# Kernel optimization log

Hardware: AMD Instinct MI355X
Metric: run time of the kernel (lower is better)

## Reference

```python
import jax, jax.numpy as jnp
import numpy as np

TOTAL = 131072          # total sentences
DIM = 690               # relation_dim (PCNN: 3*230)
NUM_CLASSES = 53        # NYT-10 relations
TOTAL_TYPE = 324        # type_num^2 = 18^2
NUM_BAGS = 8192
ALPHA = 0.9


def setup_inputs() -> dict:
    key = jax.random.key(0)
    ks = jax.random.split(key, 8)
    x = jax.random.normal(ks[0], (TOTAL, DIM), dtype=jnp.float32)
    # strictly increasing bag boundaries: scope[0]=0, scope[-1]=TOTAL, all bags non-empty
    rng = np.random.default_rng(0)
    cuts = np.sort(rng.choice(np.arange(1, TOTAL), NUM_BAGS - 1, replace=False))
    input_scope = jnp.asarray(np.concatenate([[0], cuts, [TOTAL]]), dtype=jnp.int32)
    type_label = jax.random.randint(ks[1], (TOTAL,), 0, TOTAL_TYPE, dtype=jnp.int32)
    query = jax.random.randint(ks[2], (TOTAL,), 0, NUM_CLASSES, dtype=jnp.int32)
    # learned parameters (xavier-ish scale)
    rel_scale = (6.0 / (NUM_CLASSES + DIM)) ** 0.5
    typ_scale = (6.0 / (TOTAL_TYPE + DIM)) ** 0.5
    lin_scale = (6.0 / (DIM + TOTAL_TYPE)) ** 0.5
    relation_weight = jax.random.uniform(ks[3], (NUM_CLASSES, DIM), jnp.float32, -rel_scale, rel_scale)
    type_weight = jax.random.uniform(ks[4], (TOTAL_TYPE, DIM), jnp.float32, -typ_scale, typ_scale)
    bias = jax.random.normal(ks[5], (NUM_CLASSES,), dtype=jnp.float32)
    liner_w = jax.random.uniform(ks[6], (TOTAL_TYPE, DIM), jnp.float32, -lin_scale, lin_scale)
    liner_b = jnp.zeros((TOTAL_TYPE,), dtype=jnp.float32)
    return {
        "x": x, "input_scope": input_scope, "type_label": type_label, "query": query,
        "relation_weight": relation_weight, "type_weight": type_weight, "bias": bias,
        "liner_w": liner_w, "liner_b": liner_b,
    }


def reference(x, input_scope, type_label, query, relation_weight, type_weight, bias, liner_w, liner_b):
    # ---- soft_type (beta != 0 branch) ----
    type_logits = jax.nn.softmax(x @ liner_w.T + liner_b, axis=1)          # [total, T2]
    max_scores = jnp.max(type_logits, axis=1, keepdims=True)               # [total, 1]
    one_hot = jax.nn.one_hot(type_label, TOTAL_TYPE, dtype=type_logits.dtype)
    nscore = type_logits + ALPHA * max_scores * one_hot
    soft_label = jnp.argmax(nscore, axis=1)                                # [total]

    # ---- _train_logits: per-sentence attention logits ----
    xt = x + type_weight[soft_label]                                       # [total, D]
    att = jnp.sum(xt * relation_weight[query], axis=1)                     # [total]

    # ---- bag-wise segment softmax + weighted sum over scopes ----
    seg = jnp.searchsorted(input_scope, jnp.arange(TOTAL), side="right") - 1  # [total] bag ids
    m = jax.ops.segment_max(att, seg, num_segments=NUM_BAGS)               # [bags]
    p = jnp.exp(att - m[seg])
    s = jax.ops.segment_sum(p, seg, num_segments=NUM_BAGS)                 # [bags]
    score = p / s[seg]                                                     # [total]
    bag_repre = jax.ops.segment_sum(score[:, None] * x, seg, num_segments=NUM_BAGS)  # [bags, D]

    # ---- _logits ----
    logits = bag_repre @ relation_weight.T + bias                          # [bags, C]
    return logits, type_logits
```

## Files before the change

kernel.cpp:

```cpp
#include <hip/hip_runtime.h>
#include <hip/hip_bf16.h>

#define TOTAL   131072
#define DIMK    690
#define KPAD    704
#define KSTEPS  22
#define NCLASS  53
#define NTYPE   324
#define NCOLS   377
#define NPAD    384
#define NBAGS   8192
#define ALPHA   0.9f
#define TAU     1e-5f
#define FLAGCAP 32768
#define ZS      388

typedef short  bf16x8 __attribute__((ext_vector_type(8)));
typedef float  f32x4  __attribute__((ext_vector_type(4)));

__device__ __forceinline__ unsigned short bf16_rne(float f) {
    unsigned int u = __float_as_uint(f);
    u = (u + 0x7fffu + ((u >> 16) & 1u)) >> 16;
    return (unsigned short)u;
}
__device__ __forceinline__ float bf16f(unsigned short h) {
    return __uint_as_float(((unsigned int)h) << 16);
}

__global__ __launch_bounds__(256) void k_pack(const float* __restrict__ liner_w,
                                              const float* __restrict__ rel_w,
                                              unsigned short* __restrict__ whP,
                                              unsigned short* __restrict__ wlP) {
    const int id = blockIdx.x * 256 + threadIdx.x;
    if (id >= NPAD * KPAD) return;
    const int n = id / KPAD, k = id % KPAD;
    float v = 0.f;
    if (k < DIMK) {
        if (n < NTYPE)      v = liner_w[(size_t)n * DIMK + k];
        else if (n < NCOLS) v = rel_w[(size_t)(n - NTYPE) * DIMK + k];
    }
    const unsigned short hi = bf16_rne(v);
    const unsigned short lo = bf16_rne(v - bf16f(hi));
    const int t = n >> 4, col = n & 15, s = k >> 5, kk = k & 31;
    const int lane = (kk >> 3) * 16 + col, j = kk & 7;
    const int pidx = ((t * KSTEPS + s) * 64 + lane) * 8 + j;
    whP[pidx] = hi;
    wlP[pidx] = lo;
}

__global__ __launch_bounds__(256) void k_table(const float* __restrict__ tw,
                                               const float* __restrict__ rw,
                                               float* __restrict__ table) {
    const int pair = blockIdx.x * 4 + (threadIdx.x >> 6);
    const int lane = threadIdx.x & 63;
    if (pair >= NTYPE * NCLASS) return;
    const int s = pair / NCLASS;
    const int q = pair % NCLASS;
    const float* a = tw + (size_t)s * DIMK;
    const float* b = rw + (size_t)q * DIMK;
    float acc = 0.f;
    for (int k = lane; k < DIMK; k += 64) acc += a[k] * b[k];
#pragma unroll
    for (int off = 32; off; off >>= 1) acc += __shfl_xor(acc, off);
    if (lane == 0) table[pair] = acc;
}

template<int MT>
__device__ __forceinline__ void epi_chunk(f32x4 (&acc)[4][6],
                                          float* __restrict__ zS,
                                          const float* __restrict__ sB,
                                          const int* __restrict__ type_label,
                                          const int* __restrict__ query,
                                          const float* __restrict__ table,
                                          float* __restrict__ type_logits,
                                          float* __restrict__ att,
                                          float* __restrict__ xr,
                                          int* __restrict__ flagcnt,
                                          int* __restrict__ flaglist,
                                          int base, int wv, int ln) {
    __syncthreads();
#pragma unroll
    for (int nt = 0; nt < 6; ++nt) {
        const int colb = wv * 96 + nt * 16 + (ln & 15);
        const float bb = sB[colb];
#pragma unroll
        for (int rg = 0; rg < 4; ++rg) {
            const int rl = (ln >> 4) * 4 + rg;
            zS[rl * ZS + colb] = acc[MT][nt][rg] + bb;
        }
    }
    __syncthreads();

    for (int rr = 0; rr < 4; ++rr) {
        const int rl   = wv * 4 + rr;
        const int grow = base + MT * 16 + rl;
        const float* zrow = &zS[rl * ZS];

        float m = -INFINITY;
#pragma unroll
        for (int j = 0; j < 6; ++j) {
            const int c = ln + 64 * j;
            if (c < NTYPE) m = fmaxf(m, zrow[c]);
        }
#pragma unroll
        for (int off = 32; off; off >>= 1) m = fmaxf(m, __shfl_xor(m, off));

        float e[6];
        float ssum = 0.f;
#pragma unroll
        for (int j = 0; j < 6; ++j) {
            const int c = ln + 64 * j;
            e[j] = 0.f;
            if (c < NTYPE) { e[j] = __expf(zrow[c] - m); ssum += e[j]; }
        }
#pragma unroll
        for (int off = 32; off; off >>= 1) ssum += __shfl_xor(ssum, off);
        const float inv = 1.0f / ssum;

        const int label = type_label[grow];
        float bestv = -INFINITY;
        int   besti = NTYPE;
#pragma unroll
        for (int j = 0; j < 6; ++j) {
            const int c = ln + 64 * j;
            if (c < NTYPE) {
                const float p = e[j] * inv;
                type_logits[(size_t)grow * NTYPE + c] = p;
                const float v = p + ((c == label) ? ALPHA * inv : 0.f);
                if (v > bestv || (v == bestv && c < besti)) { bestv = v; besti = c; }
            }
        }
#pragma unroll
        for (int off = 32; off; off >>= 1) {
            const float ov = __shfl_xor(bestv, off);
            const int   oi = __shfl_xor(besti, off);
            if (ov > bestv || (ov == bestv && oi < besti)) { bestv = ov; besti = oi; }
        }

        float sv = -INFINITY;
#pragma unroll
        for (int j = 0; j < 6; ++j) {
            const int c = ln + 64 * j;
            if (c < NTYPE && c != besti) {
                const float v = e[j] * inv + ((c == label) ? ALPHA * inv : 0.f);
                sv = fmaxf(sv, v);
            }
        }
#pragma unroll
        for (int off = 32; off; off >>= 1) sv = fmaxf(sv, __shfl_xor(sv, off));

        const int q = query[grow];
        if (ln == 0) {
            att[grow] = zrow[NTYPE + q] + table[besti * NCLASS + q];
            if (bestv - sv < TAU) {
                const int ix = atomicAdd(flagcnt, 1);
                if (ix < FLAGCAP) flaglist[ix] = grow;
            }
        }
        if (ln < NCLASS)
            xr[(size_t)grow * NCLASS + ln] = zrow[NTYPE + ln];
    }
}

__global__ __launch_bounds__(256, 2) void k_main(const float* __restrict__ x,
                                                 const int* __restrict__ type_label,
                                                 const int* __restrict__ query,
                                                 const unsigned short* __restrict__ whP,
                                                 const unsigned short* __restrict__ wlP,
                                                 const float* __restrict__ liner_b,
                                                 const float* __restrict__ table,
                                                 float* __restrict__ type_logits,
                                                 float* __restrict__ att,
                                                 float* __restrict__ xr,
                                                 int* __restrict__ flagcnt,
                                                 int* __restrict__ flaglist) {
    __shared__ unsigned short aS[2][2][2048];
    __shared__ float zS[16 * ZS];
    __shared__ float sB[NPAD];

    const int tid  = threadIdx.x;
    const int base = blockIdx.x * 64;
    const int wv   = tid >> 6;
    const int ln   = tid & 63;

    const int srow  = tid >> 2;
    const int kpart = tid & 3;

    f32x4 acc[4][6];
#pragma unroll
    for (int mt = 0; mt < 4; ++mt)
#pragma unroll
        for (int nt = 0; nt < 6; ++nt)
            acc[mt][nt] = (f32x4){0.f, 0.f, 0.f, 0.f};

    float xv[8];
    auto load_x = [&](int s, float* dst) {
        const int k0 = s * 32 + kpart * 8;
        const float* xp = x + (size_t)(base + srow) * DIMK + k0;
        if (k0 + 8 <= DIMK) {
            const float2 p0 = *(const float2*)(xp + 0);
            const float2 p1 = *(const float2*)(xp + 2);
            const float2 p2 = *(const float2*)(xp + 4);
            const float2 p3 = *(const float2*)(xp + 6);
            dst[0] = p0.x; dst[1] = p0.y; dst[2] = p1.x; dst[3] = p1.y;
            dst[4] = p2.x; dst[5] = p2.y; dst[6] = p3.x; dst[7] = p3.y;
        } else {
#pragma unroll
            for (int j = 0; j < 8; ++j) dst[j] = (k0 + j < DIMK) ? xp[j] : 0.f;
        }
    };
    auto write_a = [&](int nb, const float* src) {
        const int widx = (kpart * 64 + srow) * 8;
        bf16x8 hv, lv;
#pragma unroll
        for (int j = 0; j < 8; ++j) {
            const unsigned short h = bf16_rne(src[j]);
            hv[j] = (short)h;
            lv[j] = (short)bf16_rne(src[j] - bf16f(h));
        }
        *(bf16x8*)&aS[nb][0][widx] = hv;
        *(bf16x8*)&aS[nb][1][widx] = lv;
    };

    load_x(0, xv);
    write_a(0, xv);
    for (int c = tid; c < NPAD; c += 256) sB[c] = (c < NTYPE) ? liner_b[c] : 0.f;
    __syncthreads();

    const int aidx_base = ((ln >> 4) * 64 + (ln & 15)) * 8;
    for (int s = 0; s < KSTEPS; ++s) {
        const int cur = s & 1;
        float xn[8];
        if (s + 1 < KSTEPS) load_x(s + 1, xn);

        bf16x8 ah[4], al[4];
#pragma unroll
        for (int mt = 0; mt < 4; ++mt) {
            const int aidx = aidx_base + mt * 128;
            ah[mt] = *(const bf16x8*)&aS[cur][0][aidx];
            al[mt] = *(const bf16x8*)&aS[cur][1][aidx];
        }
#pragma unroll
        for (int nt = 0; nt < 6; ++nt) {
            const int ntg = wv * 6 + nt;
            const size_t boff = ((size_t)(ntg * KSTEPS + s) * 64 + ln) * 8;
            const bf16x8 bh = *(const bf16x8*)(whP + boff);
            const bf16x8 bl = *(const bf16x8*)(wlP + boff);
#pragma unroll
            for (int mt = 0; mt < 4; ++mt) {
                acc[mt][nt] = __builtin_amdgcn_mfma_f32_16x16x32_bf16(ah[mt], bh, acc[mt][nt], 0, 0, 0);
                acc[mt][nt] = __builtin_amdgcn_mfma_f32_16x16x32_bf16(ah[mt], bl, acc[mt][nt], 0, 0, 0);
                acc[mt][nt] = __builtin_amdgcn_mfma_f32_16x16x32_bf16(al[mt], bh, acc[mt][nt], 0, 0, 0);
            }
        }
        if (s + 1 < KSTEPS) write_a(1 - cur, xn);
        __syncthreads();
    }

    epi_chunk<0>(acc, zS, sB, type_label, query, table, type_logits, att, xr,
                 flagcnt, flaglist, base, wv, ln);
    epi_chunk<1>(acc, zS, sB, type_label, query, table, type_logits, att, xr,
                 flagcnt, flaglist, base, wv, ln);
    epi_chunk<2>(acc, zS, sB, type_label, query, table, type_logits, att, xr,
                 flagcnt, flaglist, base, wv, ln);
    epi_chunk<3>(acc, zS, sB, type_label, query, table, type_logits, att, xr,
                 flagcnt, flaglist, base, wv, ln);
}

__global__ __launch_bounds__(256) void k_fix(const float* __restrict__ x,
                                             const float* __restrict__ liner_w,
                                             const float* __restrict__ liner_b,
                                             const int* __restrict__ type_label,
                                             const int* __restrict__ query,
                                             const float* __restrict__ table,
                                             const float* __restrict__ xr,
                                             const int* __restrict__ flagcnt,
                                             const int* __restrict__ flaglist,
                                             float* __restrict__ att) {
    __shared__ float xs[704];
    __shared__ float zs[NTYPE];
    __shared__ float redm[4];
    __shared__ float redv[4];
    __shared__ int   redi[4];
    const int tid = threadIdx.x;
    const int wv  = tid >> 6;
    const int ln  = tid & 63;
    int count = *flagcnt;
    if (count > FLAGCAP) count = FLAGCAP;

    for (int f = blockIdx.x; f < count; f += gridDim.x) {
        const int row = flaglist[f];
        __syncthreads();
        for (int k = tid; k < 704; k += 256) xs[k] = (k < DIMK) ? x[(size_t)row * DIMK + k] : 0.f;
        __syncthreads();

        for (int ci = 0; ci < 81; ++ci) {
            const int c = wv * 81 + ci;
            const float* w = liner_w + (size_t)c * DIMK;
            float acc = 0.f;
#pragma unroll
            for (int kk = 0; kk < 11; ++kk) {
                const int k = ln + kk * 64;
                const float wval = (k < DIMK) ? w[k] : 0.f;
                acc = fmaf(xs[k], wval, acc);
            }
#pragma unroll
            for (int off = 32; off; off >>= 1) acc += __shfl_xor(acc, off);
            if (ln == 0) zs[c] = acc + liner_b[c];
        }
        __syncthreads();

        float z0 = (tid < NTYPE) ? zs[tid] : -INFINITY;
        const int c1 = tid + 256;
        float z1 = (c1 < NTYPE) ? zs[c1] : -INFINITY;
        float m = fmaxf(z0, z1);
#pragma unroll
        for (int off = 32; off; off >>= 1) m = fmaxf(m, __shfl_xor(m, off));
        if (ln == 0) redm[wv] = m;
        __syncthreads();
        m = fmaxf(fmaxf(redm[0], redm[1]), fmaxf(redm[2], redm[3]));

        const int label = type_label[row];
        const float u0 = (tid < NTYPE) ? (__expf(z0 - m) + ((tid == label) ? ALPHA : 0.f)) : -1.f;
        const float u1 = (c1 < NTYPE)  ? (__expf(z1 - m) + ((c1 == label) ? ALPHA : 0.f))  : -1.f;
        float bv = u0; int bi = tid;
        if (u1 > bv) { bv = u1; bi = c1; }
#pragma unroll
        for (int off = 32; off; off >>= 1) {
            const float ov = __shfl_xor(bv, off);
            const int   oi = __shfl_xor(bi, off);
            if (ov > bv || (ov == bv && oi < bi)) { bv = ov; bi = oi; }
        }
        if (ln == 0) { redv[wv] = bv; redi[wv] = bi; }
        __syncthreads();
        if (tid == 0) {
            float fbv = redv[0]; int fbi = redi[0];
#pragma unroll
            for (int w = 1; w < 4; ++w) {
                if (redv[w] > fbv || (redv[w] == fbv && redi[w] < fbi)) {
                    fbv = redv[w]; fbi = redi[w];
                }
            }
            const int q = query[row];
            att[row] = xr[(size_t)row * NCLASS + q] + table[fbi * NCLASS + q];
        }
    }
}

__global__ __launch_bounds__(64) void k_bag(const float* __restrict__ att,
                                            const float* __restrict__ xr,
                                            const int* __restrict__ scope,
                                            const float* __restrict__ bias,
                                            float* __restrict__ logits) {
    const int b = blockIdx.x;
    const int lane = threadIdx.x;
    const int s0 = scope[b];
    const int s1 = scope[b + 1];

    float m = -INFINITY;
    for (int i = s0 + lane; i < s1; i += 64) m = fmaxf(m, att[i]);
#pragma unroll
    for (int off = 32; off; off >>= 1) m = fmaxf(m, __shfl_xor(m, off));

    float sum = 0.f;
    float acc = 0.f;
    for (int i0 = s0; i0 < s1; i0 += 64) {
        const int n = min(64, s1 - i0);
        float e = 0.f;
        if (lane < n) e = __expf(att[i0 + lane] - m);
        float es = e;
#pragma unroll
        for (int off = 32; off; off >>= 1) es += __shfl_xor(es, off);
        sum += es;
        for (int j = 0; j < n; ++j) {
            const float ej = __shfl(e, j);
            if (lane < NCLASS) acc = fmaf(ej, xr[(size_t)(i0 + j) * NCLASS + lane], acc);
        }
    }
    const float inv = 1.0f / sum;
    if (lane < NCLASS) logits[b * NCLASS + lane] = acc * inv + bias[lane];
}

extern "C" void kernel_launch(void* const* d_in, const int* in_sizes, int n_in,
                              void* d_out, int out_size, void* d_ws, size_t ws_size,
                              hipStream_t stream) {
    const float* x          = (const float*)d_in[0];
    const int*   scope      = (const int*)d_in[1];
    const int*   type_label = (const int*)d_in[2];
    const int*   query      = (const int*)d_in[3];
    const float* rel_w      = (const float*)d_in[4];
    const float* type_w     = (const float*)d_in[5];
    const float* bias       = (const float*)d_in[6];
    const float* liner_w    = (const float*)d_in[7];
    const float* liner_b    = (const float*)d_in[8];

    float* logits      = (float*)d_out;
    float* type_logits = (float*)d_out + NBAGS * NCLASS;

    float* ws = (float*)d_ws;
    float*          table    = ws;
    float*          att      = ws + 17408;
    float*          xr       = ws + 148480;
    unsigned short* whP      = (unsigned short*)(ws + 7095296);
    unsigned short* wlP      = (unsigned short*)(ws + 7230464);
    int*            flagcnt  = (int*)(ws + 7365632);
    int*            flaglist = (int*)(ws + 7365633);

    hipMemsetAsync(flagcnt, 0, sizeof(int), stream);
    hipLaunchKernelGGL(k_pack, dim3((NPAD * KPAD + 255) / 256), dim3(256), 0, stream,
                       liner_w, rel_w, whP, wlP);
    hipLaunchKernelGGL(k_table, dim3((NTYPE * NCLASS + 3) / 4), dim3(256), 0, stream,
                       type_w, rel_w, table);
    hipLaunchKernelGGL(k_main, dim3(TOTAL / 64), dim3(256), 0, stream,
                       x, type_label, query, whP, wlP, liner_b, table,
                       type_logits, att, xr, flagcnt, flaglist);
    hipLaunchKernelGGL(k_fix, dim3(1024), dim3(256), 0, stream,
                       x, liner_w, liner_b, type_label, query, table, xr,
                       flagcnt, flaglist, att);
    hipLaunchKernelGGL(k_bag, dim3(NBAGS), dim3(64), 0, stream,
                       att, xr, scope, bias, logits);
}
```

Measured before the change: 469.7 us.

## Deepen GEMM software pipeline: prefetch x two steps ahead and B fragments one step ahead

After: 482.5 us. 2.7% more time.

```diff
diff --git a/kernel.cpp b/kernel.cpp
--- a/kernel.cpp
+++ b/kernel.cpp
@@ -193,8 +193,7 @@
         for (int nt = 0; nt < 6; ++nt)
             acc[mt][nt] = (f32x4){0.f, 0.f, 0.f, 0.f};
 
-    float xv[8];
-    auto load_x = [&](int s, float* dst) {
+    auto load_x = [&](int s, float (&dst)[8]) {
         const int k0 = s * 32 + kpart * 8;
         const float* xp = x + (size_t)(base + srow) * DIMK + k0;
         if (k0 + 8 <= DIMK) {
@@ -209,7 +208,7 @@
             for (int j = 0; j < 8; ++j) dst[j] = (k0 + j < DIMK) ? xp[j] : 0.f;
         }
     };
-    auto write_a = [&](int nb, const float* src) {
+    auto write_a = [&](int nb, const float (&src)[8]) {
         const int widx = (kpart * 64 + srow) * 8;
         bf16x8 hv, lv;
 #pragma unroll
@@ -221,17 +220,35 @@
         *(bf16x8*)&aS[nb][0][widx] = hv;
         *(bf16x8*)&aS[nb][1][widx] = lv;
     };
-
-    load_x(0, xv);
-    write_a(0, xv);
+    auto loadB = [&](int s, bf16x8 (&bh)[6], bf16x8 (&bl)[6]) {
+#pragma unroll
+        for (int nt = 0; nt < 6; ++nt) {
+            const int ntg = wv * 6 + nt;
+            const size_t boff = ((size_t)(ntg * KSTEPS + s) * 64 + ln) * 8;
+            bh[nt] = *(const bf16x8*)(whP + boff);
+            bl[nt] = *(const bf16x8*)(wlP + boff);
+        }
+    };
+
+    float  xvA[8], xvB[8];
+    bf16x8 bhA[6], blA[6], bhB[6], blB[6];
+
+    load_x(0, xvA);
+    write_a(0, xvA);
+    load_x(1, xvB);
+    loadB(0, bhA, blA);
     for (int c = tid; c < NPAD; c += 256) sB[c] = (c < NTYPE) ? liner_b[c] : 0.f;
-    __syncthreads();
+    asm volatile("s_waitcnt lgkmcnt(0)" ::: "memory");
+    __builtin_amdgcn_s_barrier();
 
     const int aidx_base = ((ln >> 4) * 64 + (ln & 15)) * 8;
-    for (int s = 0; s < KSTEPS; ++s) {
-        const int cur = s & 1;
-        float xn[8];
-        if (s + 1 < KSTEPS) load_x(s + 1, xn);
+
+    auto kstep = [&](int s, int cur,
+                     float (&xw)[8], float (&xl)[8],
+                     bf16x8 (&bhC)[6], bf16x8 (&blC)[6],
+                     bf16x8 (&bhN)[6], bf16x8 (&blN)[6]) {
+        if (s + 2 < KSTEPS) load_x(s + 2, xl);
+        if (s + 1 < KSTEPS) loadB(s + 1, bhN, blN);
 
         bf16x8 ah[4], al[4];
 #pragma unroll
@@ -242,19 +259,21 @@
         }
 #pragma unroll
         for (int nt = 0; nt < 6; ++nt) {
-            const int ntg = wv * 6 + nt;
-            const size_t boff = ((size_t)(ntg * KSTEPS + s) * 64 + ln) * 8;
-            const bf16x8 bh = *(const bf16x8*)(whP + boff);
-            const bf16x8 bl = *(const bf16x8*)(wlP + boff);
 #pragma unroll
             for (int mt = 0; mt < 4; ++mt) {
-                acc[mt][nt] = __builtin_amdgcn_mfma_f32_16x16x32_bf16(ah[mt], bh, acc[mt][nt], 0, 0, 0);
-                acc[mt][nt] = __builtin_amdgcn_mfma_f32_16x16x32_bf16(ah[mt], bl, acc[mt][nt], 0, 0, 0);
-                acc[mt][nt] = __builtin_amdgcn_mfma_f32_16x16x32_bf16(al[mt], bh, acc[mt][nt], 0, 0, 0);
-            }
-        }
-        if (s + 1 < KSTEPS) write_a(1 - cur, xn);
-        __syncthreads();
+                acc[mt][nt] = __builtin_amdgcn_mfma_f32_16x16x32_bf16(ah[mt], bhC[nt], acc[mt][nt], 0, 0, 0);
+                acc[mt][nt] = __builtin_amdgcn_mfma_f32_16x16x32_bf16(ah[mt], blC[nt], acc[mt][nt], 0, 0, 0);
+                acc[mt][nt] = __builtin_amdgcn_mfma_f32_16x16x32_bf16(al[mt], bhC[nt], acc[mt][nt], 0, 0, 0);
+            }
+        }
+        if (s + 1 < KSTEPS) write_a(1 - cur, xw);
+        asm volatile("s_waitcnt lgkmcnt(0)" ::: "memory");
+        __builtin_amdgcn_s_barrier();
+    };
+
+    for (int s2 = 0; s2 < KSTEPS; s2 += 2) {
+        kstep(s2,     0, xvB, xvA, bhA, blA, bhB, blB);
+        kstep(s2 + 1, 1, xvA, xvB, bhB, blB, bhA, blA);
     }
 
     epi_chunk<0>(acc, zS, sB, type_label, query, table, type_logits, att, xr,
```

## Split fused GEMM+softmax epilogue into separate GEMM and epilogue kernels

Applied to the files above, without the earlier changes.

Result: slower. 953.6 us (+103.0%).

```diff
diff --git a/kernel.cpp b/kernel.cpp
--- a/kernel.cpp
+++ b/kernel.cpp
@@ -13,7 +13,6 @@
 #define ALPHA   0.9f
 #define TAU     1e-5f
 #define FLAGCAP 32768
-#define ZS      388
 
 typedef short  bf16x8 __attribute__((ext_vector_type(8)));
 typedef float  f32x4  __attribute__((ext_vector_type(4)));
@@ -65,117 +64,13 @@
     if (lane == 0) table[pair] = acc;
 }
 
-template<int MT>
-__device__ __forceinline__ void epi_chunk(f32x4 (&acc)[4][6],
-                                          float* __restrict__ zS,
-                                          const float* __restrict__ sB,
-                                          const int* __restrict__ type_label,
-                                          const int* __restrict__ query,
-                                          const float* __restrict__ table,
-                                          float* __restrict__ type_logits,
-                                          float* __restrict__ att,
-                                          float* __restrict__ xr,
-                                          int* __restrict__ flagcnt,
-                                          int* __restrict__ flaglist,
-                                          int base, int wv, int ln) {
-    __syncthreads();
-#pragma unroll
-    for (int nt = 0; nt < 6; ++nt) {
-        const int colb = wv * 96 + nt * 16 + (ln & 15);
-        const float bb = sB[colb];
-#pragma unroll
-        for (int rg = 0; rg < 4; ++rg) {
-            const int rl = (ln >> 4) * 4 + rg;
-            zS[rl * ZS + colb] = acc[MT][nt][rg] + bb;
-        }
-    }
-    __syncthreads();
-
-    for (int rr = 0; rr < 4; ++rr) {
-        const int rl   = wv * 4 + rr;
-        const int grow = base + MT * 16 + rl;
-        const float* zrow = &zS[rl * ZS];
-
-        float m = -INFINITY;
-#pragma unroll
-        for (int j = 0; j < 6; ++j) {
-            const int c = ln + 64 * j;
-            if (c < NTYPE) m = fmaxf(m, zrow[c]);
-        }
-#pragma unroll
-        for (int off = 32; off; off >>= 1) m = fmaxf(m, __shfl_xor(m, off));
-
-        float e[6];
-        float ssum = 0.f;
-#pragma unroll
-        for (int j = 0; j < 6; ++j) {
-            const int c = ln + 64 * j;
-            e[j] = 0.f;
-            if (c < NTYPE) { e[j] = __expf(zrow[c] - m); ssum += e[j]; }
-        }
-#pragma unroll
-        for (int off = 32; off; off >>= 1) ssum += __shfl_xor(ssum, off);
-        const float inv = 1.0f / ssum;
-
-        const int label = type_label[grow];
-        float bestv = -INFINITY;
-        int   besti = NTYPE;
-#pragma unroll
-        for (int j = 0; j < 6; ++j) {
-            const int c = ln + 64 * j;
-            if (c < NTYPE) {
-                const float p = e[j] * inv;
-                type_logits[(size_t)grow * NTYPE + c] = p;
-                const float v = p + ((c == label) ? ALPHA * inv : 0.f);
-                if (v > bestv || (v == bestv && c < besti)) { bestv = v; besti = c; }
-            }
-        }
-#pragma unroll
-        for (int off = 32; off; off >>= 1) {
-            const float ov = __shfl_xor(bestv, off);
-            const int   oi = __shfl_xor(besti, off);
-            if (ov > bestv || (ov == bestv && oi < besti)) { bestv = ov; besti = oi; }
-        }
-
-        float sv = -INFINITY;
-#pragma unroll
-        for (int j = 0; j < 6; ++j) {
-            const int c = ln + 64 * j;
-            if (c < NTYPE && c != besti) {
-                const float v = e[j] * inv + ((c == label) ? ALPHA * inv : 0.f);
-                sv = fmaxf(sv, v);
-            }
-        }
-#pragma unroll
-        for (int off = 32; off; off >>= 1) sv = fmaxf(sv, __shfl_xor(sv, off));
-
-        const int q = query[grow];
-        if (ln == 0) {
-            att[grow] = zrow[NTYPE + q] + table[besti * NCLASS + q];
-            if (bestv - sv < TAU) {
-                const int ix = atomicAdd(flagcnt, 1);
-                if (ix < FLAGCAP) flaglist[ix] = grow;
-            }
-        }
-        if (ln < NCLASS)
-            xr[(size_t)grow * NCLASS + ln] = zrow[NTYPE + ln];
-    }
-}
-
-__global__ __launch_bounds__(256, 2) void k_main(const float* __restrict__ x,
-                                                 const int* __restrict__ type_label,
-                                                 const int* __restrict__ query,
+__global__ __launch_bounds__(256, 4) void k_gemm(const float* __restrict__ x,
                                                  const unsigned short* __restrict__ whP,
                                                  const unsigned short* __restrict__ wlP,
                                                  const float* __restrict__ liner_b,
-                                                 const float* __restrict__ table,
-                                                 float* __restrict__ type_logits,
-                                                 float* __restrict__ att,
-                                                 float* __restrict__ xr,
-                                                 int* __restrict__ flagcnt,
-                                                 int* __restrict__ flaglist) {
+                                                 float* __restrict__ zt,
+                                                 float* __restrict__ xr) {
     __shared__ unsigned short aS[2][2][2048];
-    __shared__ float zS[16 * ZS];
     __shared__ float sB[NPAD];
 
     const int tid  = threadIdx.x;
@@ -193,8 +88,7 @@
         for (int nt = 0; nt < 6; ++nt)
             acc[mt][nt] = (f32x4){0.f, 0.f, 0.f, 0.f};
 
-    float xv[8];
-    auto load_x = [&](int s, float* dst) {
+    auto load_x = [&](int s, float (&dst)[8]) {
         const int k0 = s * 32 + kpart * 8;
         const float* xp = x + (size_t)(base + srow) * DIMK + k0;
         if (k0 + 8 <= DIMK) {
@@ -209,7 +103,7 @@
             for (int j = 0; j < 8; ++j) dst[j] = (k0 + j < DIMK) ? xp[j] : 0.f;
         }
     };
-    auto write_a = [&](int nb, const float* src) {
+    auto write_a = [&](int nb, const float (&src)[8]) {
         const int widx = (kpart * 64 + srow) * 8;
         bf16x8 hv, lv;
 #pragma unroll
@@ -222,10 +116,12 @@
         *(bf16x8*)&aS[nb][1][widx] = lv;
     };
 
+    float xv[8];
     load_x(0, xv);
     write_a(0, xv);
     for (int c = tid; c < NPAD; c += 256) sB[c] = (c < NTYPE) ? liner_b[c] : 0.f;
-    __syncthreads();
+    asm volatile("s_waitcnt lgkmcnt(0)" ::: "memory");
+    __builtin_amdgcn_s_barrier();
 
     const int aidx_base = ((ln >> 4) * 64 + (ln & 15)) * 8;
     for (int s = 0; s < KSTEPS; ++s) {
@@ -254,17 +150,108 @@
             }
         }
         if (s + 1 < KSTEPS) write_a(1 - cur, xn);
-        __syncthreads();
-    }
-
-    epi_chunk<0>(acc, zS, sB, type_label, query, table, type_logits, att, xr,
-                 flagcnt, flaglist, base, wv, ln);
-    epi_chunk<1>(acc, zS, sB, type_label, query, table, type_logits, att, xr,
-                 flagcnt, flaglist, base, wv, ln);
-    epi_chunk<2>(acc, zS, sB, type_label, query, table, type_logits, att, xr,
-                 flagcnt, flaglist, base, wv, ln);
-    epi_chunk<3>(acc, zS, sB, type_label, query, table, type_logits, att, xr,
-                 flagcnt, flaglist, base, wv, ln);
+        asm volatile("s_waitcnt lgkmcnt(0)" ::: "memory");
+        __builtin_amdgcn_s_barrier();
+    }
+
+#pragma unroll
+    for (int nt = 0; nt < 6; ++nt) {
+        const int col = wv * 96 + nt * 16 + (ln & 15);
+        const float bb = sB[col];
+        const int r0 = base + (ln >> 4) * 4;
+#pragma unroll
+        for (int mt = 0; mt < 4; ++mt) {
+            const int row = r0 + mt * 16;
+            if (col < NTYPE) {
+#pragma unroll
+                for (int rg = 0; rg < 4; ++rg)
+                    zt[(size_t)(row + rg) * NTYPE + col] = acc[mt][nt][rg] + bb;
+            } else if (col < NCOLS) {
+#pragma unroll
+                for (int rg = 0; rg < 4; ++rg)
+                    xr[(size_t)(row + rg) * NCLASS + (col - NTYPE)] = acc[mt][nt][rg];
+            }
+        }
+    }
+}
+
+__global__ __launch_bounds__(256) void k_epi(float* __restrict__ type_logits,
+                                             const float* __restrict__ xr,
+                                             const int* __restrict__ type_label,
+                                             const int* __restrict__ query,
+                                             const float* __restrict__ table,
+                                             float* __restrict__ att,
+                                             int* __restrict__ flagcnt,
+                                             int* __restrict__ flaglist) {
+    const int row = blockIdx.x * 4 + (threadIdx.x >> 6);
+    const int ln  = threadIdx.x & 63;
+    float* zrow = type_logits + (size_t)row * NTYPE;
+
+    float z[6];
+#pragma unroll
+    for (int j = 0; j < 6; ++j) {
+        const int c = ln + 64 * j;
+        z[j] = (c < NTYPE) ? zrow[c] : -INFINITY;
+    }
+
+    float m = -INFINITY;
+#pragma unroll
+    for (int j = 0; j < 6; ++j) m = fmaxf(m, z[j]);
+#pragma unroll
+    for (int off = 32; off; off >>= 1) m = fmaxf(m, __shfl_xor(m, off));
+
+    float e[6];
+    float ssum = 0.f;
+#pragma unroll
+    for (int j = 0; j < 6; ++j) {
+        const int c = ln + 64 * j;
+        e[j] = 0.f;
+        if (c < NTYPE) { e[j] = __expf(z[j] - m); ssum += e[j]; }
+    }
+#pragma unroll
+    for (int off = 32; off; off >>= 1) ssum += __shfl_xor(ssum, off);
+    const float inv = 1.0f / ssum;
+
+    const int label = type_label[row];
+    float bestv = -INFINITY;
+    int   besti = NTYPE;
+#pragma unroll
+    for (int j = 0; j < 6; ++j) {
+        const int c = ln + 64 * j;
+        if (c < NTYPE) {
+            const float p = e[j] * inv;
+            zrow[c] = p;
+            const float v = p + ((c == label) ? ALPHA * inv : 0.f);
+            if (v > bestv || (v == bestv && c < besti)) { bestv = v; besti = c; }
+        }
+    }
+#pragma unroll
+    for (int off = 32; off; off >>= 1) {
+        const float ov = __shfl_xor(bestv, off);
+        const int   oi = __shfl_xor(besti, off);
+        if (ov > bestv || (ov == bestv && oi < besti)) { bestv = ov; besti = oi; }
+    }
+
+    float sv = -INFINITY;
+#pragma unroll
+    for (int j = 0; j < 6; ++j) {
+        const int c = ln + 64 * j;
+        if (c < NTYPE && c != besti) {
+            const float v = e[j] * inv + ((c == label) ? ALPHA * inv : 0.f);
+            sv = fmaxf(sv, v);
+        }
+    }
+#pragma unroll
+    for (int off = 32; off; off >>= 1) sv = fmaxf(sv, __shfl_xor(sv, off));
+
+    if (ln == 0) {
+        const int q = query[row];
+        att[row] = xr[(size_t)row * NCLASS + q] + table[besti * NCLASS + q];
+        if (bestv - sv < TAU) {
+            const int ix = atomicAdd(flagcnt, 1);
+            if (ix < FLAGCAP) flaglist[ix] = row;
+        }
+    }
 }
 
 __global__ __launch_bounds__(256) void k_fix(const float* __restrict__ x,
@@ -411,9 +398,11 @@
                        liner_w, rel_w, whP, wlP);
     hipLaunchKernelGGL(k_table, dim3((NTYPE * NCLASS + 3) / 4), dim3(256), 0, stream,
                        type_w, rel_w, table);
-    hipLaunchKernelGGL(k_main, dim3(TOTAL / 64), dim3(256), 0, stream,
-                       x, type_label, query, whP, wlP, liner_b, table,
-                       type_logits, att, xr, flagcnt, flaglist);
+    hipLaunchKernelGGL(k_gemm, dim3(TOTAL / 64), dim3(256), 0, stream,
+                       x, whP, wlP, liner_b, type_logits, xr);
+    hipLaunchKernelGGL(k_epi, dim3(TOTAL / 4), dim3(256), 0, stream,
+                       type_logits, xr, type_label, query, table, att,
+                       flagcnt, flaglist);
     hipLaunchKernelGGL(k_fix, dim3(1024), dim3(256), 0, stream,
                        x, liner_w, liner_b, type_label, query, table, xr,
                        flagcnt, flaglist, att);
```

## Split k_main across 8 waves with smaller per-wave tiles and LDS-aliased epilogue

Applied to the files above, without the earlier changes.

New measurement: 438.4 us (median of 3 runs). 6.7% less time.

```diff
diff --git a/kernel.cpp b/kernel.cpp
--- a/kernel.cpp
+++ b/kernel.cpp
@@ -15,6 +15,7 @@
 #define FLAGCAP 32768
 #define ZS      388
 
+typedef short  bf16x4 __attribute__((ext_vector_type(4)));
 typedef short  bf16x8 __attribute__((ext_vector_type(8)));
 typedef float  f32x4  __attribute__((ext_vector_type(4)));
 
@@ -65,104 +66,112 @@
     if (lane == 0) table[pair] = acc;
 }
 
-template<int MT>
-__device__ __forceinline__ void epi_chunk(f32x4 (&acc)[4][6],
-                                          float* __restrict__ zS,
-                                          const float* __restrict__ sB,
-                                          const int* __restrict__ type_label,
-                                          const int* __restrict__ query,
-                                          const float* __restrict__ table,
-                                          float* __restrict__ type_logits,
-                                          float* __restrict__ att,
-                                          float* __restrict__ xr,
-                                          int* __restrict__ flagcnt,
-                                          int* __restrict__ flaglist,
-                                          int base, int wv, int ln) {
-    __syncthreads();
-#pragma unroll
-    for (int nt = 0; nt < 6; ++nt) {
-        const int colb = wv * 96 + nt * 16 + (ln & 15);
-        const float bb = sB[colb];
-#pragma unroll
-        for (int rg = 0; rg < 4; ++rg) {
-            const int rl = (ln >> 4) * 4 + rg;
-            zS[rl * ZS + colb] = acc[MT][nt][rg] + bb;
-        }
-    }
-    __syncthreads();
-
-    for (int rr = 0; rr < 4; ++rr) {
-        const int rl   = wv * 4 + rr;
-        const int grow = base + MT * 16 + rl;
-        const float* zrow = &zS[rl * ZS];
-
-        float m = -INFINITY;
-#pragma unroll
-        for (int j = 0; j < 6; ++j) {
-            const int c = ln + 64 * j;
-            if (c < NTYPE) m = fmaxf(m, zrow[c]);
-        }
-#pragma unroll
-        for (int off = 32; off; off >>= 1) m = fmaxf(m, __shfl_xor(m, off));
-
-        float e[6];
-        float ssum = 0.f;
-#pragma unroll
-        for (int j = 0; j < 6; ++j) {
-            const int c = ln + 64 * j;
-            e[j] = 0.f;
-            if (c < NTYPE) { e[j] = __expf(zrow[c] - m); ssum += e[j]; }
-        }
-#pragma unroll
-        for (int off = 32; off; off >>= 1) ssum += __shfl_xor(ssum, off);
-        const float inv = 1.0f / ssum;
-
-        const int label = type_label[grow];
-        float bestv = -INFINITY;
-        int   besti = NTYPE;
-#pragma unroll
-        for (int j = 0; j < 6; ++j) {
-            const int c = ln + 64 * j;
-            if (c < NTYPE) {
-                const float p = e[j] * inv;
-                type_logits[(size_t)grow * NTYPE + c] = p;
-                const float v = p + ((c == label) ? ALPHA * inv : 0.f);
-                if (v > bestv || (v == bestv && c < besti)) { bestv = v; besti = c; }
-            }
-        }
-#pragma unroll
-        for (int off = 32; off; off >>= 1) {
-            const float ov = __shfl_xor(bestv, off);
-            const int   oi = __shfl_xor(besti, off);
-            if (ov > bestv || (ov == bestv && oi < besti)) { bestv = ov; besti = oi; }
-        }
-
-        float sv = -INFINITY;
-#pragma unroll
-        for (int j = 0; j < 6; ++j) {
-            const int c = ln + 64 * j;
-            if (c < NTYPE && c != besti) {
-                const float v = e[j] * inv + ((c == label) ? ALPHA * inv : 0.f);
-                sv = fmaxf(sv, v);
-            }
-        }
-#pragma unroll
-        for (int off = 32; off; off >>= 1) sv = fmaxf(sv, __shfl_xor(sv, off));
-
-        const int q = query[grow];
-        if (ln == 0) {
-            att[grow] = zrow[NTYPE + q] + table[besti * NCLASS + q];
-            if (bestv - sv < TAU) {
-                const int ix = atomicAdd(flagcnt, 1);
-                if (ix < FLAGCAP) flaglist[ix] = grow;
-            }
-        }
-        if (ln < NCLASS)
-            xr[(size_t)grow * NCLASS + ln] = zrow[NTYPE + ln];
-    }
-}
-
-__global__ __launch_bounds__(256, 2) void k_main(const float* __restrict__ x,
+template<int H>
+__device__ __forceinline__ void epi8(f32x4 (&acc)[4][3],
+                                     float* __restrict__ zS,
+                                     const float* __restrict__ sB,
+                                     const int* __restrict__ type_label,
+                                     const int* __restrict__ query,
+                                     const float* __restrict__ table,
+                                     float* __restrict__ type_logits,
+                                     float* __restrict__ att,
+                                     float* __restrict__ xr,
+                                     int* __restrict__ flagcnt,
+                                     int* __restrict__ flaglist,
+                                     int base, int wv, int ln) {
+    constexpr int MT = H >> 1;
+    constexpr int Q0 = (H & 1) * 2;
+    const int q = ln >> 4;
+
+    if (q == Q0 || q == Q0 + 1) {
+        const int lr0 = (q - Q0) * 4;
+#pragma unroll
+        for (int nt = 0; nt < 3; ++nt) {
+            const int col = wv * 48 + nt * 16 + (ln & 15);
+            const float bb = sB[col];
+#pragma unroll
+            for (int rg = 0; rg < 4; ++rg)
+                zS[(lr0 + rg) * ZS + col] = acc[MT][nt][rg] + bb;
+        }
+    }
+    asm volatile("s_waitcnt lgkmcnt(0)" ::: "memory");
+    __builtin_amdgcn_s_barrier();
+
+    const int grow = base + H * 8 + wv;
+    const float* zrow = &zS[wv * ZS];
+
+    float z[6];
+#pragma unroll
+    for (int j = 0; j < 6; ++j) {
+        const int c = ln + 64 * j;
+        z[j] = (c < NTYPE) ? zrow[c] : -INFINITY;
+    }
+    float m = -INFINITY;
+#pragma unroll
+    for (int j = 0; j < 6; ++j) m = fmaxf(m, z[j]);
+#pragma unroll
+    for (int off = 32; off; off >>= 1) m = fmaxf(m, __shfl_xor(m, off));
+
+    float e[6];
+    float ssum = 0.f;
+#pragma unroll
+    for (int j = 0; j < 6; ++j) {
+        const int c = ln + 64 * j;
+        e[j] = 0.f;
+        if (c < NTYPE) { e[j] = __expf(z[j] - m); ssum += e[j]; }
+    }
+#pragma unroll
+    for (int off = 32; off; off >>= 1) ssum += __shfl_xor(ssum, off);
+    const float inv = 1.0f / ssum;
+
+    const int label = type_label[grow];
+    float bestv = -INFINITY;
+    int   besti = NTYPE;
+#pragma unroll
+    for (int j = 0; j < 6; ++j) {
+        const int c = ln + 64 * j;
+        if (c < NTYPE) {
+            const float p = e[j] * inv;
+            type_logits[(size_t)grow * NTYPE + c] = p;
+            const float v = p + ((c == label) ? ALPHA * inv : 0.f);
+            if (v > bestv || (v == bestv && c < besti)) { bestv = v; besti = c; }
+        }
+    }
+#pragma unroll
+    for (int off = 32; off; off >>= 1) {
+        const float ov = __shfl_xor(bestv, off);
+        const int   oi = __shfl_xor(besti, off);
+        if (ov > bestv || (ov == bestv && oi < besti)) { bestv = ov; besti = oi; }
+    }
+
+    float sv = -INFINITY;
+#pragma unroll
+    for (int j = 0; j < 6; ++j) {
+        const int c = ln + 64 * j;
+        if (c < NTYPE && c != besti) {
+            const float v = e[j] * inv + ((c == label) ? ALPHA * inv : 0.f);
+            sv = fmaxf(sv, v);
+        }
+    }
+#pragma unroll
+    for (int off = 32; off; off >>= 1) sv = fmaxf(sv, __shfl_xor(sv, off));
+
+    if (ln == 0) {
+        const int qq = query[grow];
+        att[grow] = zrow[NTYPE + qq] + table[besti * NCLASS + qq];
+        if (bestv - sv < TAU) {
+            const int ix = atomicAdd(flagcnt, 1);
+            if (ix < FLAGCAP) flaglist[ix] = grow;
+        }
+    }
+    if (ln < NCLASS)
+        xr[(size_t)grow * NCLASS + ln] = zrow[NTYPE + ln];
+
+    asm volatile("s_waitcnt lgkmcnt(0)" ::: "memory");
+    __builtin_amdgcn_s_barrier();
+}
+
+__global__ __launch_bounds__(512, 4) void k_main(const float* __restrict__ x,
                                                  const int* __restrict__ type_label,
                                                  const int* __restrict__ query,
                                                  const unsigned short* __restrict__ whP,
@@ -175,7 +184,6 @@
                                                  int* __restrict__ flagcnt,
                                                  int* __restrict__ flaglist) {
     __shared__ unsigned short aS[2][2][2048];
-    __shared__ float zS[16 * ZS];
     __shared__ float sB[NPAD];
 
     const int tid  = threadIdx.x;
@@ -183,54 +191,53 @@
     const int wv   = tid >> 6;
     const int ln   = tid & 63;
 
-    const int srow  = tid >> 2;
-    const int kpart = tid & 3;
-
-    f32x4 acc[4][6];
+    const int srow  = tid >> 3;
+    const int kpart = tid & 7;
+
+    f32x4 acc[4][3];
 #pragma unroll
     for (int mt = 0; mt < 4; ++mt)
 #pragma unroll
-        for (int nt = 0; nt < 6; ++nt)
+        for (int nt = 0; nt < 3; ++nt)
             acc[mt][nt] = (f32x4){0.f, 0.f, 0.f, 0.f};
 
-    float xv[8];
-    auto load_x = [&](int s, float* dst) {
-        const int k0 = s * 32 + kpart * 8;
+    auto load_x = [&](int s, float (&dst)[4]) {
+        const int k0 = s * 32 + kpart * 4;
         const float* xp = x + (size_t)(base + srow) * DIMK + k0;
-        if (k0 + 8 <= DIMK) {
+        if (k0 + 4 <= DIMK) {
             const float2 p0 = *(const float2*)(xp + 0);
             const float2 p1 = *(const float2*)(xp + 2);
-            const float2 p2 = *(const float2*)(xp + 4);
-            const float2 p3 = *(const float2*)(xp + 6);
             dst[0] = p0.x; dst[1] = p0.y; dst[2] = p1.x; dst[3] = p1.y;
-            dst[4] = p2.x; dst[5] = p2.y; dst[6] = p3.x; dst[7] = p3.y;
         } else {
 #pragma unroll
-            for (int j = 0; j < 8; ++j) dst[j] = (k0 + j < DIMK) ? xp[j] : 0.f;
+            for (int j = 0; j < 4; ++j) dst[j] = (k0 + j < DIMK) ? xp[j] : 0.f;
         }
     };
-    auto write_a = [&](int nb, const float* src) {
-        const int widx = (kpart * 64 + srow) * 8;
-        bf16x8 hv, lv;
-#pragma unroll
-        for (int j = 0; j < 8; ++j) {
+    auto write_a = [&](int nb, const float (&src)[4]) {
+        const int kb = kpart >> 1, j0 = (kpart & 1) * 4;
+        const int widx = (kb * 64 + srow) * 8 + j0;
+        bf16x4 hv, lv;
+#pragma unroll
+        for (int j = 0; j < 4; ++j) {
             const unsigned short h = bf16_rne(src[j]);
             hv[j] = (short)h;
             lv[j] = (short)bf16_rne(src[j] - bf16f(h));
         }
-        *(bf16x8*)&aS[nb][0][widx] = hv;
-        *(bf16x8*)&aS[nb][1][widx] = lv;
+        *(bf16x4*)&aS[nb][0][widx] = hv;
+        *(bf16x4*)&aS[nb][1][widx] = lv;
     };
 
+    float xv[4];
     load_x(0, xv);
     write_a(0, xv);
-    for (int c = tid; c < NPAD; c += 256) sB[c] = (c < NTYPE) ? liner_b[c] : 0.f;
-    __syncthreads();
+    for (int c = tid; c < NPAD; c += 512) sB[c] = (c < NTYPE) ? liner_b[c] : 0.f;
+    asm volatile("s_waitcnt lgkmcnt(0)" ::: "memory");
+    __builtin_amdgcn_s_barrier();
 
     const int aidx_base = ((ln >> 4) * 64 + (ln & 15)) * 8;
     for (int s = 0; s < KSTEPS; ++s) {
         const int cur = s & 1;
-        float xn[8];
+        float xn[4];
         if (s + 1 < KSTEPS) load_x(s + 1, xn);
 
         bf16x8 ah[4], al[4];
@@ -241,8 +248,8 @@
             al[mt] = *(const bf16x8*)&aS[cur][1][aidx];
         }
 #pragma unroll
-        for (int nt = 0; nt < 6; ++nt) {
-            const int ntg = wv * 6 + nt;
+        for (int nt = 0; nt < 3; ++nt) {
+            const int ntg = wv * 3 + nt;
             const size_t boff = ((size_t)(ntg * KSTEPS + s) * 64 + ln) * 8;
             const bf16x8 bh = *(const bf16x8*)(whP + boff);
             const bf16x8 bl = *(const bf16x8*)(wlP + boff);
@@ -254,17 +261,19 @@
             }
         }
         if (s + 1 < KSTEPS) write_a(1 - cur, xn);
-        __syncthreads();
-    }
-
-    epi_chunk<0>(acc, zS, sB, type_label, query, table, type_logits, att, xr,
-                 flagcnt, flaglist, base, wv, ln);
-    epi_chunk<1>(acc, zS, sB, type_label, query, table, type_logits, att, xr,
-                 flagcnt, flaglist, base, wv, ln);
-    epi_chunk<2>(acc, zS, sB, type_label, query, table, type_logits, att, xr,
-                 flagcnt, flaglist, base, wv, ln);
-    epi_chunk<3>(acc, zS, sB, type_label, query, table, type_logits, att, xr,
-                 flagcnt, flaglist, base, wv, ln);
+        asm volatile("s_waitcnt lgkmcnt(0)" ::: "memory");
+        __builtin_amdgcn_s_barrier();
+    }
+
+    float* zS = (float*)aS;
+    epi8<0>(acc, zS, sB, type_label, query, table, type_logits, att, xr, flagcnt, flaglist, base, wv, ln);
+    epi8<1>(acc, zS, sB, type_label, query, table, type_logits, att, xr, flagcnt, flaglist, base, wv, ln);
+    epi8<2>(acc, zS, sB, type_label, query, table, type_logits, att, xr, flagcnt, flaglist, base, wv, ln);
+    epi8<3>(acc, zS, sB, type_label, query, table, type_logits, att, xr, flagcnt, flaglist, base, wv, ln);
+    epi8<4>(acc, zS, sB, type_label, query, table, type_logits, att, xr, flagcnt, flaglist, base, wv, ln);
+    epi8<5>(acc, zS, sB, type_label, query, table, type_logits, att, xr, flagcnt, flaglist, base, wv, ln);
+    epi8<6>(acc, zS, sB, type_label, query, table, type_logits, att, xr, flagcnt, flaglist, base, wv, ln);
+    epi8<7>(acc, zS, sB, type_label, query, table, type_logits, att, xr, flagcnt, flaglist, base, wv, ln);
 }
 
 __global__ __launch_bounds__(256) void k_fix(const float* __restrict__ x,
@@ -411,7 +420,7 @@
                        liner_w, rel_w, whP, wlP);
     hipLaunchKernelGGL(k_table, dim3((NTYPE * NCLASS + 3) / 4), dim3(256), 0, stream,
                        type_w, rel_w, table);
-    hipLaunchKernelGGL(k_main, dim3(TOTAL / 64), dim3(256), 0, stream,
+    hipLaunchKernelGGL(k_main, dim3(TOTAL / 64), dim3(512), 0, stream,
                        x, type_label, query, whP, wlP, liner_b, table,
                        type_logits, att, xr, flagcnt, flaglist);
     hipLaunchKernelGGL(k_fix, dim3(1024), dim3(256), 0, stream,
```
